# Performance work log

Measured on AMD Instinct MI355X. Metric: run time of the kernel, lower is better.

## Reference

```python
import jax, jax.numpy as jnp
import numpy as np

N_ATOMS = 128
BATCH = 512


def _build_buffers(n):
    # Segments: all non-adjacent bond pairs (i,i+1,j,j+1), j >= i+2, j+1 <= n-1.
    segs = np.array([(i, i + 1, j, j + 1)
                     for i in range(n - 3)
                     for j in range(i + 2, n - 1)], dtype=np.int32)  # (S,4)

    def pidx(a, b):  # linear index of pair (a,b), a<b, in row-major triu(offset=1) order
        return a * n - a * (a + 1) // 2 + (b - a - 1)

    # Each writhe value scatters into its 4 incident residue pairs.
    # Pairs (0,1) [triu idx 0] and (n-2,n-1) [last triu idx] are never incident,
    # so ranks among interior pairs are (triu idx - 1); they are re-inserted by pad.
    inc = []
    for (i, _, j, _) in segs:
        for (a, b) in ((i, j), (i, j + 1), (i + 1, j), (i + 1, j + 1)):
            inc.append(pidx(a, b) - 1)
    indices = np.array(inc, dtype=np.int32)  # (4*S,)

    # Sort permutation placing [upper-triu values, lower-triu values] into
    # row-major order of all off-diagonal (r,c) entries, keyed by r*n + c.
    iu = np.stack(np.triu_indices(n, 1))  # (2, P) row-major
    vals = np.concatenate([iu[0] * n + iu[1], iu[1] * n + iu[0]])
    sort = np.argsort(vals).astype(np.int32)  # (n^2 - n,)
    return segs, indices, sort


def setup_inputs() -> dict:
    key = jax.random.key(0)
    xyz = jax.random.normal(key, (BATCH, N_ATOMS, 3), dtype=jnp.float32)
    segs, indices, sort = _build_buffers(N_ATOMS)
    return {
        "xyz": xyz,
        "segments": jnp.asarray(segs),
        "indices": jnp.asarray(indices),
        "sort": jnp.asarray(sort),
    }


def _divnorm(x):
    return x / jnp.linalg.norm(x, axis=-1, keepdims=True)


def _writhe(xyz, segments):
    # xyz: (B,N,3); segments: (S,4) -> writhe per segment pair, (B,S)
    B, S = xyz.shape[0], segments.shape[0]
    p = xyz[:, segments]  # (B,S,4,3) gathered endpoints [s1a,s1b,s2a,s2b]
    # d[k] = normalize(p_{2+j} - p_i), k = 2*i + j  (the 4 inter-segment directions)
    d = _divnorm((p[:, :, None, 2:, :] - p[:, :, :2, None, :]).reshape(B, S, 4, 3))
    axial = jnp.cross(p[:, :, 3] - p[:, :, 2], p[:, :, 1] - p[:, :, 0])  # (B,S,3)
    signs = jnp.sign(jnp.sum(axial * d[:, :, 0], -1))  # (B,S)
    # 4 face normals of the spherical quadrilateral, then Gauss-Bonnet angle sum
    nrm = _divnorm(jnp.cross(d[:, :, jnp.array([0, 1, 3, 2])],
                             d[:, :, jnp.array([1, 3, 2, 0])]))  # (B,S,4,3)
    cosang = jnp.clip(jnp.sum(nrm * nrm[:, :, jnp.array([1, 2, 3, 0])], -1), -1.0, 1.0)
    omega = jnp.arcsin(cosang).sum(-1)  # (B,S)
    return omega * signs / (2.0 * jnp.pi)


def _laplacian(wr, indices, sort, n):
    # wr: (B,S); scatter-add each writhe into its 4 incident residue pairs,
    # pad back the two untouched pairs, symmetrize, and sort into row-major
    # off-diagonal order -> (B, n^2 - n)
    M = (n * n - n) // 2 - 2
    triu = jnp.zeros((wr.shape[0], M), wr.dtype).at[:, indices].add(
        jnp.repeat(wr, 4, axis=1))
    padded = jnp.pad(triu, ((0, 0), (1, 1)))
    return jnp.concatenate([padded, padded], axis=1)[:, sort]


def reference(xyz, segments, indices, sort):
    xyz = xyz.reshape(-1, N_ATOMS, 3)
    wr = _writhe(xyz, segments)
    return _laplacian(wr, indices, sort, N_ATOMS)
```

## Files before the change

kernel.cpp:

```cpp
#include <hip/hip_runtime.h>
#include <math.h>

#define NATOMS    128
#define NSEG      7875
#define NSEG_PAD  8192
#define NPAIR     8128
#define OUT_PER_B 16256
#define BLOCK     1024

typedef float v2f __attribute__((ext_vector_type(2)));
__device__ __forceinline__ v2f mk2(float a, float b) { v2f r; r.x = a; r.y = b; return r; }

struct P3 { v2f x, y, z; };
__device__ __forceinline__ P3 psub(P3 a, P3 b) { return {a.x - b.x, a.y - b.y, a.z - b.z}; }
__device__ __forceinline__ P3 pcross(P3 a, P3 b) {
    return {a.y * b.z - a.z * b.y, a.z * b.x - a.x * b.z, a.x * b.y - a.y * b.x};
}
__device__ __forceinline__ v2f pdot(P3 a, P3 b) { return a.x * b.x + a.y * b.y + a.z * b.z; }
__device__ __forceinline__ v2f prsq(v2f q) {
    v2f r; r.x = __builtin_amdgcn_rsqf(q.x); r.y = __builtin_amdgcn_rsqf(q.y); return r;
}
__device__ __forceinline__ v2f pclip1(v2f x) {
    return __builtin_elementwise_min(__builtin_elementwise_max(x, mk2(-1.f, -1.f)),
                                     mk2(1.f, 1.f));
}

__device__ __forceinline__ v2f fast_asin2(v2f x) {
    v2f a = __builtin_elementwise_abs(x);
    v2f p = mk2(-0.0187293f, -0.0187293f);
    p = p * a + mk2( 0.0742610f,  0.0742610f);
    p = p * a + mk2(-0.2121144f, -0.2121144f);
    p = p * a + mk2( 1.5707288f,  1.5707288f);
    v2f om = mk2(1.0f, 1.0f) - a;
    v2f sq; sq.x = __builtin_amdgcn_sqrtf(om.x); sq.y = __builtin_amdgcn_sqrtf(om.y);
    v2f r = mk2(1.57079632679f, 1.57079632679f) - sq * p;
    return __builtin_elementwise_copysign(r, x);
}

__device__ __forceinline__ int seg_row_base(int i) { return 125 * i - (__umul24(i, i - 1) >> 1); }
__device__ __forceinline__ int pair_row_base(int a) { return (__umul24(a, 255 - a) >> 1); }

__device__ __forceinline__ v2f seg_writhe_pair(unsigned pa, unsigned pb,
                                               const float* sx, const float* sy,
                                               const float* sz) {
    int jA = (int)(pa & 127u), iA = (int)(pa >> 7);
    int jB = (int)(pb & 127u), iB = (int)(pb >> 7);

    P3 p0 = {mk2(sx[iA],     sx[iB]),     mk2(sy[iA],     sy[iB]),     mk2(sz[iA],     sz[iB])};
    P3 p1 = {mk2(sx[iA + 1], sx[iB + 1]), mk2(sy[iA + 1], sy[iB + 1]), mk2(sz[iA + 1], sz[iB + 1])};
    P3 p2 = {mk2(sx[jA],     sx[jB]),     mk2(sy[jA],     sy[jB]),     mk2(sz[jA],     sz[jB])};
    P3 p3 = {mk2(sx[jA + 1], sx[jB + 1]), mk2(sy[jA + 1], sy[jB + 1]), mk2(sz[jA + 1], sz[jB + 1])};

    P3 u0 = psub(p2, p0);
    P3 u1 = psub(p3, p0);
    P3 u2 = psub(p2, p1);
    P3 u3 = psub(p3, p1);

    P3 n0 = pcross(u0, u1);
    P3 n1 = pcross(u1, u3);
    P3 n2 = pcross(u3, u2);
    P3 n3 = pcross(u2, u0);

    v2f q0 = pdot(n0, n0);
    v2f q1 = pdot(n1, n1);
    v2f q2 = pdot(n2, n2);
    v2f q3 = pdot(n3, n3);

    v2f c0 = pclip1(pdot(n0, n1) * prsq(q0 * q1));
    v2f c1 = pclip1(pdot(n1, n2) * prsq(q1 * q2));
    v2f c2 = pclip1(pdot(n2, n3) * prsq(q2 * q3));
    v2f c3 = pclip1(pdot(n3, n0) * prsq(q3 * q0));

    v2f sd = pdot(n2, u0);
    v2f omega = fast_asin2(c0) + fast_asin2(c1) + fast_asin2(c2) + fast_asin2(c3);

    v2f sgn;
    sgn.x = (sd.x > 0.f) ? -1.f : ((sd.x < 0.f) ? 1.f : 0.f);
    sgn.y = (sd.y > 0.f) ? -1.f : ((sd.y < 0.f) ? 1.f : 0.f);

    return omega * sgn * mk2(0.15915494309189535f, 0.15915494309189535f);
}

__global__ __launch_bounds__(BLOCK, 8) void writhe_fused(
    const float* __restrict__ xyz,
    float*       __restrict__ out)
{
    __shared__ float sx[NATOMS], sy[NATOMS], sz[NATOMS];
    __shared__ float swr[NSEG_PAD];
    __shared__ unsigned short sidx[NSEG_PAD];
    __shared__ unsigned short spair[NPAIR];

    const int b = blockIdx.x;
    const int t = threadIdx.x;

    if (t < 3 * NATOMS) {
        float v = xyz[(size_t)b * (3 * NATOMS) + t];
        int a = t / 3, c = t - 3 * a;
        if (c == 0) sx[a] = v; else if (c == 1) sy[a] = v; else sz[a] = v;
    }

    {
        int s = t * 8;
        if (s < NSEG) {
            int i = (int)((251.0f - __builtin_amdgcn_sqrtf(63001.0f - 8.0f * (float)s)) * 0.5f);
            i = max(i, 0);
            i += (seg_row_base(i + 1) <= s);
            i += (seg_row_base(i + 1) <= s);
            i -= (seg_row_base(i) > s);
            i -= (seg_row_base(i) > s);
            int j = s - seg_row_base(i) + i + 2;
            #pragma unroll
            for (int k = 0; k < 8; ++k) {
                if (s < NSEG) sidx[s] = (unsigned short)((i << 7) | j);
                ++s; ++j;
                if (j > 126) { ++i; j = i + 2; }
            }
        }
        if (t < NSEG_PAD - NSEG) sidx[NSEG + t] = (unsigned short)((124 << 7) | 126);
    }
    {
        int p = t * 8;
        if (p < NPAIR) {
            int a = (int)((255.0f - __builtin_amdgcn_sqrtf(65025.0f - 8.0f * (float)p)) * 0.5f);
            a = max(a, 0);
            a += (pair_row_base(a + 1) <= p);
            a += (pair_row_base(a + 1) <= p);
            a -= (pair_row_base(a) > p);
            a -= (pair_row_base(a) > p);
            int bb = a + 1 + (p - pair_row_base(a));
            #pragma unroll
            for (int k = 0; k < 8; ++k) {
                if (p < NPAIR) spair[p] = (unsigned short)((a << 7) | bb);
                ++p; ++bb;
                if (bb > 127) { ++a; bb = a + 1; }
            }
        }
    }
    __syncthreads();

    #pragma unroll
    for (int g = 0; g < 2; ++g) {
        const int sA = g * 4096 + t;
        v2f w1 = seg_writhe_pair(sidx[sA],        sidx[sA + 1024], sx, sy, sz);
        v2f w2 = seg_writhe_pair(sidx[sA + 2048], sidx[sA + 3072], sx, sy, sz);
        swr[sA]        = w1.x;
        swr[sA + 1024] = w1.y;
        swr[sA + 2048] = w2.x;
        swr[sA + 3072] = w2.y;
    }
    __syncthreads();

    float* ob = out + (size_t)b * OUT_PER_B;
    for (int p = t; p < NPAIR; p += BLOCK) {
        unsigned pk = spair[p];
        int bb = (int)(pk & 127u);
        int a  = (int)(pk >> 7);

        int am1 = a - 1;
        int s00 = 125 * am1 - ((am1 * (am1 - 1)) >> 1) + bb - a - 2;
        int s10 = s00 + 125 - a;

        bool v00 = (a >= 1) && (a <= 125) && (bb >= a + 2);
        bool v01 = (a >= 1) && (a <= 125) && (bb <= 126);
        bool v10 = (a <= 124) && (bb >= a + 3);
        bool v11 = (a <= 124) && (bb <= 126) && (bb >= a + 2);

        int c00 = min(max(s00,     0), NSEG - 1);
        int c01 = min(max(s00 + 1, 0), NSEG - 1);
        int c10 = min(max(s10,     0), NSEG - 1);
        int c11 = min(max(s10 + 1, 0), NSEG - 1);

        float sum = (v00 ? swr[c00] : 0.0f) + (v01 ? swr[c01] : 0.0f)
                  + (v10 ? swr[c10] : 0.0f) + (v11 ? swr[c11] : 0.0f);

        int k1 = 127 * a + bb - 1;
        int k2 = 127 * bb + a;
        ob[k1] = sum;
        ob[k2] = sum;
    }
}

extern "C" void kernel_launch(void* const* d_in, const int* in_sizes, int n_in,
                              void* d_out, int out_size, void* d_ws, size_t ws_size,
                              hipStream_t stream) {
    const float* xyz = (const float*)d_in[0];
    float*       out = (float*)d_out;

    int B = in_sizes[0] / (NATOMS * 3);
    writhe_fused<<<B, BLOCK, 0, stream>>>(xyz, out);
}
```

Baseline: 92.03 us.

## Write output row-major with float4 stores and halve block size

The output phase now iterates over output positions in row-major order and computes each (row, col) with a magic-multiply division. Each thread stores four contiguous floats with a single float4 write, replacing the two scattered scalar stores per pair (one of them transposed). The shared pair-index table is removed, and the block shrinks to 512 threads, each handling twice the segments. The intent is coalesced, vectorized global writes and less LDS setup work. The cost is recomputing the segment sum for both symmetric entries and per-element index arithmetic.

Measured after the change: 91.58 us. Within noise of the previous version (-0.5%).

```diff
diff --git a/kernel.cpp b/kernel.cpp
--- a/kernel.cpp
+++ b/kernel.cpp
@@ -6,7 +6,7 @@
 #define NSEG_PAD  8192
 #define NPAIR     8128
 #define OUT_PER_B 16256
-#define BLOCK     1024
+#define BLOCK     512
 
 typedef float v2f __attribute__((ext_vector_type(2)));
 __device__ __forceinline__ v2f mk2(float a, float b) { v2f r; r.x = a; r.y = b; return r; }
@@ -38,7 +38,6 @@
 }
 
 __device__ __forceinline__ int seg_row_base(int i) { return 125 * i - (__umul24(i, i - 1) >> 1); }
-__device__ __forceinline__ int pair_row_base(int a) { return (__umul24(a, 255 - a) >> 1); }
 
 __device__ __forceinline__ v2f seg_writhe_pair(unsigned pa, unsigned pb,
                                                const float* sx, const float* sy,
@@ -81,14 +80,13 @@
     return omega * sgn * mk2(0.15915494309189535f, 0.15915494309189535f);
 }
 
-__global__ __launch_bounds__(BLOCK, 8) void writhe_fused(
+__global__ __launch_bounds__(BLOCK, 4) void writhe_fused(
     const float* __restrict__ xyz,
     float*       __restrict__ out)
 {
     __shared__ float sx[NATOMS], sy[NATOMS], sz[NATOMS];
     __shared__ float swr[NSEG_PAD];
     __shared__ unsigned short sidx[NSEG_PAD];
-    __shared__ unsigned short spair[NPAIR];
 
     const int b = blockIdx.x;
     const int t = threadIdx.x;
@@ -100,7 +98,7 @@
     }
 
     {
-        int s = t * 8;
+        int s = t * 16;
         if (s < NSEG) {
             int i = (int)((251.0f - __builtin_amdgcn_sqrtf(63001.0f - 8.0f * (float)s)) * 0.5f);
             i = max(i, 0);
@@ -110,7 +108,7 @@
             i -= (seg_row_base(i) > s);
             int j = s - seg_row_base(i) + i + 2;
             #pragma unroll
-            for (int k = 0; k < 8; ++k) {
+            for (int k = 0; k < 16; ++k) {
                 if (s < NSEG) sidx[s] = (unsigned short)((i << 7) | j);
                 ++s; ++j;
                 if (j > 126) { ++i; j = i + 2; }
@@ -118,65 +116,52 @@
         }
         if (t < NSEG_PAD - NSEG) sidx[NSEG + t] = (unsigned short)((124 << 7) | 126);
     }
-    {
-        int p = t * 8;
-        if (p < NPAIR) {
-            int a = (int)((255.0f - __builtin_amdgcn_sqrtf(65025.0f - 8.0f * (float)p)) * 0.5f);
-            a = max(a, 0);
-            a += (pair_row_base(a + 1) <= p);
-            a += (pair_row_base(a + 1) <= p);
-            a -= (pair_row_base(a) > p);
-            a -= (pair_row_base(a) > p);
-            int bb = a + 1 + (p - pair_row_base(a));
-            #pragma unroll
-            for (int k = 0; k < 8; ++k) {
-                if (p < NPAIR) spair[p] = (unsigned short)((a << 7) | bb);
-                ++p; ++bb;
-                if (bb > 127) { ++a; bb = a + 1; }
-            }
-        }
-    }
     __syncthreads();
 
     #pragma unroll
-    for (int g = 0; g < 2; ++g) {
-        const int sA = g * 4096 + t;
-        v2f w1 = seg_writhe_pair(sidx[sA],        sidx[sA + 1024], sx, sy, sz);
-        v2f w2 = seg_writhe_pair(sidx[sA + 2048], sidx[sA + 3072], sx, sy, sz);
+    for (int g = 0; g < 4; ++g) {
+        const int sA = g * 2048 + t;
+        v2f w1 = seg_writhe_pair(sidx[sA],        sidx[sA + 512],  sx, sy, sz);
+        v2f w2 = seg_writhe_pair(sidx[sA + 1024], sidx[sA + 1536], sx, sy, sz);
         swr[sA]        = w1.x;
-        swr[sA + 1024] = w1.y;
-        swr[sA + 2048] = w2.x;
-        swr[sA + 3072] = w2.y;
+        swr[sA + 512]  = w1.y;
+        swr[sA + 1024] = w2.x;
+        swr[sA + 1536] = w2.y;
     }
     __syncthreads();
 
     float* ob = out + (size_t)b * OUT_PER_B;
-    for (int p = t; p < NPAIR; p += BLOCK) {
-        unsigned pk = spair[p];
-        int bb = (int)(pk & 127u);
-        int a  = (int)(pk >> 7);
+    for (int kq = t; kq < OUT_PER_B / 4; kq += BLOCK) {
+        const int k0 = kq << 2;
+        float acc[4];
+        #pragma unroll
+        for (int q = 0; q < 4; ++q) {
+            const int k = k0 + q;
+            const int r = (int)(((unsigned)k * 132105u) >> 24);
+            int c = k - r * 127;
+            c += (c >= r);
+            const int a  = min(r, c);
+            const int bb = max(r, c);
 
-        int am1 = a - 1;
-        int s00 = 125 * am1 - ((am1 * (am1 - 1)) >> 1) + bb - a - 2;
-        int s10 = s00 + 125 - a;
+            const int am1 = a - 1;
+            const int s00 = 125 * am1 - ((am1 * (am1 - 1)) >> 1) + bb - a - 2;
+            const int s10 = s00 + 125 - a;
 
-        bool v00 = (a >= 1) && (a <= 125) && (bb >= a + 2);
-        bool v01 = (a >= 1) && (a <= 125) && (bb <= 126);
-        bool v10 = (a <= 124) && (bb >= a + 3);
-        bool v11 = (a <= 124) && (bb <= 126) && (bb >= a + 2);
+            const bool v00 = (a >= 1) && (a <= 125) && (bb >= a + 2);
+            const bool v01 = (a >= 1) && (a <= 125) && (bb <= 126);
+            const bool v10 = (a <= 124) && (bb >= a + 3);
+            const bool v11 = (a <= 124) && (bb <= 126) && (bb >= a + 2);
 
-        int c00 = min(max(s00,     0), NSEG - 1);
-        int c01 = min(max(s00 + 1, 0), NSEG - 1);
-        int c10 = min(max(s10,     0), NSEG - 1);
-        int c11 = min(max(s10 + 1, 0), NSEG - 1);
+            const int c00 = min(max(s00,     0), NSEG - 1);
+            const int c01 = min(max(s00 + 1, 0), NSEG - 1);
+            const int c10 = min(max(s10,     0), NSEG - 1);
+            const int c11 = min(max(s10 + 1, 0), NSEG - 1);
 
-        float sum = (v00 ? swr[c00] : 0.0f) + (v01 ? swr[c01] : 0.0f)
-                  + (v10 ? swr[c10] : 0.0f) + (v11 ? swr[c11] : 0.0f);
-
-        int k1 = 127 * a + bb - 1;
-        int k2 = 127 * bb + a;
-        ob[k1] = sum;
-        ob[k2] = sum;
+            acc[q] = (v00 ? swr[c00] : 0.0f) + (v01 ? swr[c01] : 0.0f)
+                   + (v10 ? swr[c10] : 0.0f) + (v11 ? swr[c11] : 0.0f);
+        }
+        float4 res; res.x = acc[0]; res.y = acc[1]; res.z = acc[2]; res.w = acc[3];
+        *reinterpret_cast<float4*>(ob + k0) = res;
     }
 }
 
```
